# Performance work log

Measured on AMD Instinct MI355X. Metric: run time of the kernel, lower is better.

Reference implementation:

```python
import jax, jax.numpy as jnp
import numpy as np
import math

LUT_RES = 512
TWO_PI = 2.0 * math.pi
# LUT tables: sin/cos sampled uniformly over [0, 2*pi)
_SIN_TABLE = jnp.sin(jnp.arange(LUT_RES, dtype=jnp.float32) * (TWO_PI / LUT_RES))


def _lut_idx(phase):
    # phase mod 2*pi mapped to [0, LUT_RES) integer bin (floor lookup)
    frac = jnp.mod(phase, TWO_PI) * (1.0 / TWO_PI)
    return (frac * LUT_RES).astype(jnp.int32) % LUT_RES


def setup_inputs() -> dict:
    key = jax.random.key(0)
    k1, k2, k3 = jax.random.split(key, 3)
    B, S, E, N = 2, 1024, 128, 512
    x = jax.random.normal(k1, (B, S, E), dtype=jnp.float32)
    w = jax.random.normal(k2, (E, N), dtype=jnp.float32) * 0.1          # init_freq_scale
    b = jax.random.uniform(k3, (E, N), dtype=jnp.float32) * TWO_PI      # init_offset_scale
    t = jnp.arange(S, dtype=jnp.float32)
    return {"x": x, "w": w, "b": b, "t": t}


def reference(x, w, b, t):
    # phase: (B, S, E, N) = w*x (broadcast outer product) + b + t
    phase = (w[None, None, :, :] * x[:, :, :, None]
             + b[None, None, :, :]
             + t[None, :, None, None])
    sin_vals = _SIN_TABLE[_lut_idx(phase)]   # LUT sin lookup
    return sin_vals.sum(axis=2)              # reduce over embed_dim -> (B, S, N)
```

## Files before the change

### kernel.cpp

```cpp
#include <hip/hip_runtime.h>
#include <math.h>


constexpr int E_DIM = 128;
constexpr int N_DIM = 512;
constexpr int ST    = 4;

__global__ __launch_bounds__(512) void sin_layer_kernel(
    const float* __restrict__ x,
    const float* __restrict__ w,
    const float* __restrict__ bv_,
    const float* __restrict__ t,
    float* __restrict__ out,
    int S)
{
    const int n   = threadIdx.x;
    const int bs0 = blockIdx.x * ST;

    constexpr float TWO_PI_F = 6.2831854820251465f;
    constexpr float INV2PI   = 0.15915493667125702f;
    constexpr float SCALE    = 512.0f * INV2PI;
    constexpr float INV512   = 1.0f / 512.0f;

    float acc[ST];
    float ts[ST];
    const float* xrow[ST];
#pragma unroll
    for (int i = 0; i < ST; ++i) {
        acc[i] = 0.0f;
        int bs = bs0 + i;
        int s  = (bs >= S) ? (bs - S) : bs;
        ts[i]  = t[s];
        xrow[i] = x + (size_t)bs * E_DIM;
    }

#pragma unroll 4
    for (int e = 0; e < E_DIM; ++e) {
        const float wv = w[e * N_DIM + n];
        const float bb = bv_[e * N_DIM + n];
#pragma unroll
        for (int i = 0; i < ST; ++i) {
            const float xv = xrow[i][e];
            float p = __fadd_rn(__fadd_rn(__fmul_rn(wv, xv), bb), ts[i]);
            float u = p * INV2PI;
            float q = floorf(u);
            float m = __fmaf_rn(-q, TWO_PI_F, p);
            float fi   = m * SCALE;
            float fbin = truncf(fi);
            float rev  = fbin * INV512;
            acc[i] += __builtin_amdgcn_sinf(rev);
        }
    }

#pragma unroll
    for (int i = 0; i < ST; ++i) {
        out[(size_t)(bs0 + i) * N_DIM + n] = acc[i];
    }
}

extern "C" void kernel_launch(void* const* d_in, const int* in_sizes, int n_in,
                              void* d_out, int out_size, void* d_ws, size_t ws_size,
                              hipStream_t stream) {
    const float* x = (const float*)d_in[0];
    const float* w = (const float*)d_in[1];
    const float* b = (const float*)d_in[2];
    const float* t = (const float*)d_in[3];
    float* out = (float*)d_out;

    const int S  = in_sizes[3];
    const int BS = in_sizes[0] / E_DIM;

    const int grid = BS / ST;
    sin_layer_kernel<<<grid, N_DIM, 0, stream>>>(x, w, b, t, out, S);
}
```

Before: 94.77 us.

## Prescale phase by 1/2pi and use fract, split N across smaller blocks

The phase is now computed directly in revolutions: w, b and t are prescaled by 1/(2*pi), and one FMA plus a hardware fract replaces the mul/add/floor/fma/mul/trunc chain for the mod-2pi bin lookup. The launch also changes to 256-thread blocks that each cover half of N with two sequence rows, giving four times as many blocks. This cuts the ALU work per element and raises the block count, but the reassociated arithmetic can put some phases into a different bin than the reference's exact rounding order.

```diff
diff --git a/kernel.cpp b/kernel.cpp
--- a/kernel.cpp
+++ b/kernel.cpp
@@ -4,9 +4,10 @@
 
 constexpr int E_DIM = 128;
 constexpr int N_DIM = 512;
-constexpr int ST    = 4;
+constexpr int ST    = 2;
+constexpr int TPB   = 256;
 
-__global__ __launch_bounds__(512) void sin_layer_kernel(
+__global__ __launch_bounds__(TPB) void sin_layer_kernel(
     const float* __restrict__ x,
     const float* __restrict__ w,
     const float* __restrict__ bv_,
@@ -14,41 +15,40 @@
     float* __restrict__ out,
     int S)
 {
-    const int n   = threadIdx.x;
-    const int bs0 = blockIdx.x * ST;
+    constexpr float INV2PI = 0.15915493667125702f;
+    constexpr float INV512 = 1.0f / 512.0f;
 
-    constexpr float TWO_PI_F = 6.2831854820251465f;
-    constexpr float INV2PI   = 0.15915493667125702f;
-    constexpr float SCALE    = 512.0f * INV2PI;
-    constexpr float INV512   = 1.0f / 512.0f;
+    const int nh  = blockIdx.x & 1;
+    const int g   = blockIdx.x >> 1;
+    const int n   = nh * TPB + threadIdx.x;
+    const int bs0 = g * ST;
 
+    float tn[ST];
     float acc[ST];
-    float ts[ST];
     const float* xrow[ST];
 #pragma unroll
     for (int i = 0; i < ST; ++i) {
+        const int bs = bs0 + i;
+        const int s  = bs % S;
+        tn[i]  = t[s] * INV2PI;
+        xrow[i] = x + (size_t)bs * E_DIM;
         acc[i] = 0.0f;
-        int bs = bs0 + i;
-        int s  = (bs >= S) ? (bs - S) : bs;
-        ts[i]  = t[s];
-        xrow[i] = x + (size_t)bs * E_DIM;
     }
+
+    const float* wp = w   + n;
+    const float* bp = bv_ + n;
 
 #pragma unroll 4
     for (int e = 0; e < E_DIM; ++e) {
-        const float wv = w[e * N_DIM + n];
-        const float bb = bv_[e * N_DIM + n];
+        const float wn = wp[(size_t)e * N_DIM] * INV2PI;
+        const float bn = bp[(size_t)e * N_DIM] * INV2PI;
 #pragma unroll
         for (int i = 0; i < ST; ++i) {
             const float xv = xrow[i][e];
-            float p = __fadd_rn(__fadd_rn(__fmul_rn(wv, xv), bb), ts[i]);
-            float u = p * INV2PI;
-            float q = floorf(u);
-            float m = __fmaf_rn(-q, TWO_PI_F, p);
-            float fi   = m * SCALE;
-            float fbin = truncf(fi);
-            float rev  = fbin * INV512;
-            acc[i] += __builtin_amdgcn_sinf(rev);
+            float u = __fmaf_rn(wn, xv, bn + tn[i]);
+            float f = __builtin_amdgcn_fractf(u);
+            float k = floorf(f * 512.0f);
+            acc[i] += __builtin_amdgcn_sinf(k * INV512);
         }
     }
 
@@ -70,6 +70,6 @@
     const int S  = in_sizes[3];
     const int BS = in_sizes[0] / E_DIM;
 
-    const int grid = BS / ST;
-    sin_layer_kernel<<<grid, N_DIM, 0, stream>>>(x, w, b, t, out, S);
+    const int grid = (BS / ST) * (N_DIM / TPB);
+    sin_layer_kernel<<<grid, TPB, 0, stream>>>(x, w, b, t, out, S);
 }
```

After: 91.64 us. -3.3%, faster.
